# Kernel tuning notes

Measured on AMD Instinct MI355X. Metric: run time of the kernel, lower is better.

Reference implementation:

```python
import jax, jax.numpy as jnp
import numpy as np

MAX_K_QK = 64
MAX_K_V = 64
MAX_K_KNOW = 128


def threshold_gate(scores, tau, max_k):
    # scores: [B,S,N], tau: [B,S,1]
    raw = scores - tau
    gate = jnp.where(raw > 0, raw, 1e-08 * jnp.exp(raw))
    exp_gate = jnp.exp(gate) - 1.0
    k = min(max_k, scores.shape[-1])
    topk_vals, _ = jax.lax.top_k(exp_gate, k)
    threshold = topk_vals[:, :, -1:]
    exp_gate = jnp.where(exp_gate >= threshold, exp_gate, 0.0)
    gate_sum = exp_gate.sum(axis=-1, keepdims=True) + 1e-08
    gate_strength = jnp.tanh(exp_gate.max(axis=-1, keepdims=True))
    return exp_gate / gate_sum * gate_strength


def setup_inputs() -> dict:
    key = jax.random.key(0)
    ks = jax.random.split(key, 8)
    B, S, D = 2, 2048, 1024
    N_QK, N_V, N_KNOW = 4096, 4096, 8192
    scale = 0.02  # keep scores in a sane range for exp()
    return {
        "x": jax.random.normal(ks[0], (B, S, D), jnp.float32),
        "qk_emb": jax.random.normal(ks[1], (N_QK, D), jnp.float32) * scale,
        "v_emb": jax.random.normal(ks[2], (N_V, D), jnp.float32) * scale,
        "know_emb": jax.random.normal(ks[3], (N_KNOW, D), jnp.float32) * scale,
        "w_attn": jax.random.normal(ks[4], (D, 3), jnp.float32) * scale,
        "b_attn": jnp.zeros((3,), jnp.float32),
        "w_know": jax.random.normal(ks[5], (D, 1), jnp.float32) * scale,
        "b_know": jnp.zeros((1,), jnp.float32),
    }


def reference(x, qk_emb, v_emb, know_emb, w_attn, b_attn, w_know, b_know):
    # deterministic=True -> router dropout is identity
    # attention gates
    scores_qk = jnp.einsum("bsd,nd->bsn", x, qk_emb)
    scores_v = jnp.einsum("bsd,nd->bsn", x, v_emb)
    tau_all = x @ w_attn + b_attn  # [B,S,3]
    g_Q = threshold_gate(scores_qk, tau_all[:, :, 0:1], MAX_K_QK)
    g_K = threshold_gate(scores_qk, tau_all[:, :, 1:2], MAX_K_QK)
    g_V = threshold_gate(scores_v, tau_all[:, :, 2:3], MAX_K_V)
    t_qk = 1.0 / qk_emb.shape[0]
    t_v = 1.0 / v_emb.shape[0]
    aux_attn = (
        ((g_Q.mean(axis=(0, 1)) - t_qk) ** 2).sum() * g_Q.shape[-1]
        + ((g_K.mean(axis=(0, 1)) - t_qk) ** 2).sum() * g_K.shape[-1]
        + ((g_V.mean(axis=(0, 1)) - t_v) ** 2).sum() * g_V.shape[-1]
    )
    # knowledge gates
    scores_know = jnp.einsum("bsd,nd->bsn", x, know_emb)
    tau_know = x @ w_know + b_know  # [B,S,1]
    g_know = threshold_gate(scores_know, tau_know, MAX_K_KNOW)
    t_know = 1.0 / know_emb.shape[0]
    aux_know = ((g_know.mean(axis=(0, 1)) - t_know) ** 2).sum() * g_know.shape[-1]
    return (g_Q, g_K, g_V, aux_attn, g_know, aux_know)
```

## Files before the change

### kernel.cpp

```cpp
#include <hip/hip_runtime.h>
#include <hip/hip_bf16.h>


#define M_ROWS 4096
#define DIM    1024
#define N_QK   4096
#define N_KNOW 8192

typedef unsigned short ushortT;
typedef __attribute__((ext_vector_type(8)))  short short8;
typedef __attribute__((ext_vector_type(16))) float f32x16;

__global__ __launch_bounds__(256) void tau_kernel(
    const float* __restrict__ x, const float* __restrict__ w_attn,
    const float* __restrict__ b_attn, const float* __restrict__ w_know,
    const float* __restrict__ b_know, float* __restrict__ tau4, int D)
{
    __shared__ float s_f[4][4];
    const int row = blockIdx.x;
    const int tid = threadIdx.x;
    const float* xr = x + (size_t)row * D;
    float p0 = 0.f, p1 = 0.f, p2 = 0.f, p3 = 0.f;
    for (int d = tid; d < D; d += 256) {
        float xv = xr[d];
        p0 += xv * w_attn[d * 3 + 0];
        p1 += xv * w_attn[d * 3 + 1];
        p2 += xv * w_attn[d * 3 + 2];
        p3 += xv * w_know[d];
    }
#pragma unroll
    for (int o = 32; o > 0; o >>= 1) {
        p0 += __shfl_down(p0, o, 64);
        p1 += __shfl_down(p1, o, 64);
        p2 += __shfl_down(p2, o, 64);
        p3 += __shfl_down(p3, o, 64);
    }
    const int lane = tid & 63, wv = tid >> 6;
    if (lane == 0) { s_f[wv][0] = p0; s_f[wv][1] = p1; s_f[wv][2] = p2; s_f[wv][3] = p3; }
    __syncthreads();
    if (tid < 4) {
        float v = s_f[0][tid] + s_f[1][tid] + s_f[2][tid] + s_f[3][tid];
        v += (tid < 3) ? b_attn[tid] : b_know[0];
        tau4[(size_t)row * 4 + tid] = v;
    }
}

__device__ __forceinline__ void split4(const float4 v, uint2& H, uint2& L) {
    float vv[4] = {v.x, v.y, v.z, v.w};
    unsigned h[4], l[4];
#pragma unroll
    for (int i = 0; i < 4; i++) {
        __hip_bfloat16 hb = __float2bfloat16(vv[i]);
        float r = vv[i] - __bfloat162float(hb);
        __hip_bfloat16 lb = __float2bfloat16(r);
        h[i] = *(ushortT*)&hb;
        l[i] = *(ushortT*)&lb;
    }
    H.x = h[0] | (h[1] << 16); H.y = h[2] | (h[3] << 16);
    L.x = l[0] | (l[1] << 16); L.y = l[2] | (l[3] << 16);
}

__global__ __launch_bounds__(256) void convertA(
    const float* __restrict__ src, ushortT* __restrict__ dst, int nElem4)
{
    int g = blockIdx.x * 256 + threadIdx.x;
    if (g >= nElem4) return;
    int row = g >> 8;
    int c4  = g & 255;
    int chunk = c4 >> 3, pos = c4 & 7;
    const float4 v = *(const float4*)(src + (size_t)row * DIM + c4 * 4);
    uint2 H, L;
    split4(v, H, L);
    ushortT* base = dst + (size_t)row * 2048 + chunk * 64;
    *(uint2*)(base + pos * 4)      = H;
    *(uint2*)(base + 32 + pos * 4) = L;
}

__global__ __launch_bounds__(256) void gemm_fused3(
    const ushortT* __restrict__ Aext, const ushortT* __restrict__ Bext,
    float* __restrict__ gQ, float* __restrict__ gV, float* __restrict__ gKn,
    int nb0)
{
    __shared__ ushortT AHL[2][128 * 64];
    __shared__ ushortT BHL[2][128 * 64];
    const int tid = threadIdx.x;
    const int wave = tid >> 6, lane = tid & 63;
    const int l32 = lane & 31, h = lane >> 5;
    const int rx7 = l32 & 7;
    const int wm = (wave >> 1) * 64, wn = (wave & 1) * 64;
    const long long m0 = (long long)blockIdx.y * 128;
    const int nblk = nb0 + blockIdx.x;

    float* C; long long ldc; long long n0;
    if (nblk < 32)      { C = gQ;  ldc = N_QK;   n0 = (long long)nblk * 128; }
    else if (nblk < 64) { C = gV;  ldc = N_QK;   n0 = (long long)(nblk - 32) * 128; }
    else                { C = gKn; ldc = N_KNOW; n0 = (long long)(nblk - 64) * 128; }

    const ushortT* gAp[4]; const ushortT* gBp[4]; int lOff[4];
#pragma unroll
    for (int it = 0; it < 4; ++it) {
        int f = it * 256 + tid;
        int r = f >> 3, sp = f & 7;
        int sg = sp ^ (r & 7);
        gAp[it] = Aext + (m0 + r) * 2048 + sg * 8;
        gBp[it] = Bext + ((long long)blockIdx.x * 128 + r) * 2048 + sg * 8;
        lOff[it] = f * 8;
    }

    f32x16 acc[2][2] = {};

#define STAGE(buf, c) do {                                                         \
    _Pragma("unroll")                                                              \
    for (int it = 0; it < 4; ++it) {                                               \
        __builtin_amdgcn_global_load_lds(                                          \
            (const __attribute__((address_space(1))) unsigned*)(const void*)(gAp[it] + (c) * 64), \
            (__attribute__((address_space(3))) unsigned*)(void*)(&AHL[buf][0] + lOff[it]), 16, 0, 0); \
        __builtin_amdgcn_global_load_lds(                                          \
            (const __attribute__((address_space(1))) unsigned*)(const void*)(gBp[it] + (c) * 64), \
            (__attribute__((address_space(3))) unsigned*)(void*)(&BHL[buf][0] + lOff[it]), 16, 0, 0); \
    }                                                                              \
} while (0)

#define COMPUTE(buf) do {                                                          \
    _Pragma("unroll")                                                              \
    for (int kb = 0; kb < 2; ++kb) {                                               \
        const int so = ((kb * 2 + h) ^ rx7) * 16;                                  \
        short8 aH[2], aL[2], bH[2], bL[2];                                         \
        _Pragma("unroll")                                                          \
        for (int t = 0; t < 2; ++t) {                                              \
            const char* pa = (const char*)(&AHL[buf][0]) + (wm + t * 32 + l32) * 128; \
            const char* pb = (const char*)(&BHL[buf][0]) + (wn + t * 32 + l32) * 128; \
            aH[t] = *(const short8*)(pa + so);                                     \
            aL[t] = *(const short8*)(pa + (so ^ 64));                              \
            bH[t] = *(const short8*)(pb + so);                                     \
            bL[t] = *(const short8*)(pb + (so ^ 64));                              \
        }                                                                          \
        _Pragma("unroll")                                                          \
        for (int i = 0; i < 2; ++i)                                                \
            _Pragma("unroll")                                                      \
            for (int j = 0; j < 2; ++j)                                            \
                acc[i][j] = __builtin_amdgcn_mfma_f32_32x32x16_bf16(aH[i], bH[j], acc[i][j], 0, 0, 0); \
        _Pragma("unroll")                                                          \
        for (int i = 0; i < 2; ++i)                                                \
            _Pragma("unroll")                                                      \
            for (int j = 0; j < 2; ++j)                                            \
                acc[i][j] = __builtin_amdgcn_mfma_f32_32x32x16_bf16(aH[i], bL[j], acc[i][j], 0, 0, 0); \
        _Pragma("unroll")                                                          \
        for (int i = 0; i < 2; ++i)                                                \
            _Pragma("unroll")                                                      \
            for (int j = 0; j < 2; ++j)                                            \
                acc[i][j] = __builtin_amdgcn_mfma_f32_32x32x16_bf16(aL[i], bH[j], acc[i][j], 0, 0, 0); \
        _Pragma("unroll")                                                          \
        for (int i = 0; i < 2; ++i)                                                \
            _Pragma("unroll")                                                      \
            for (int j = 0; j < 2; ++j)                                            \
                acc[i][j] = __builtin_amdgcn_mfma_f32_32x32x16_bf16(aL[i], bL[j], acc[i][j], 0, 0, 0); \
    }                                                                              \
} while (0)

    STAGE(0, 0);
    __syncthreads();

    for (int c = 0; c < 32; c += 2) {
        STAGE(1, c + 1);
        COMPUTE(0);
        __syncthreads();
        if (c + 2 < 32) STAGE(0, c + 2);
        COMPUTE(1);
        __syncthreads();
    }
#undef STAGE
#undef COMPUTE

#pragma unroll
    for (int ti = 0; ti < 2; ++ti)
#pragma unroll
        for (int tj = 0; tj < 2; ++tj) {
            long long col = n0 + wn + tj * 32 + l32;
            long long rb  = m0 + wm + ti * 32 + 4 * h;
#pragma unroll
            for (int reg = 0; reg < 16; ++reg) {
                long long row = rb + (reg & 3) + 8 * (reg >> 2);
                C[row * ldc + col] = acc[ti][tj][reg];
            }
        }
}

__global__ __launch_bounds__(256) void gemm_fused2(
    const ushortT* __restrict__ Aext, const float* __restrict__ qk_emb,
    const float* __restrict__ v_emb, const float* __restrict__ know_emb,
    float* __restrict__ gQ, float* __restrict__ gV, float* __restrict__ gKn,
    long long rowOff)
{
    __shared__ ushortT AHL[128 * 64];
    __shared__ ushortT BHL[128 * 64];
    const int tid = threadIdx.x;
    const int wave = tid >> 6, lane = tid & 63;
    const int l32 = lane & 31, h = lane >> 5;
    const int rx7 = l32 & 7;
    const int wm = (wave >> 1) * 64, wn = (wave & 1) * 64;
    const long long m0 = (long long)blockIdx.y * 128;
    const int nblk = blockIdx.x;

    const float* Bsrc; float* C; long long ldc; long long n0;
    if (nblk < 32)      { Bsrc = qk_emb;   C = gQ;  ldc = N_QK;   n0 = (long long)nblk * 128; }
    else if (nblk < 64) { Bsrc = v_emb;    C = gV;  ldc = N_QK;   n0 = (long long)(nblk - 32) * 128; }
    else                { Bsrc = know_emb; C = gKn; ldc = N_KNOW; n0 = (long long)(nblk - 64) * 128; }

    const ushortT* gAp[4]; ushortT* lAp[4];
    const float*   gBp[4]; int offH[4], offL[4];
#pragma unroll
    for (int it = 0; it < 4; ++it) {
        int f = it * 256 + tid;
        int r = f >> 3, sp = f & 7;
        int sg = sp ^ (r & 7);
        gAp[it] = Aext + (m0 + r) * 2048 + sg * 8;
        lAp[it] = AHL + f * 8;
        int c4 = f & 7;
        int s = c4 >> 1, hf = c4 & 1;
        offH[it] = r * 128 + ((s ^ (r & 7)) * 16) + hf * 8;
        offL[it] = r * 128 + (((4 | s) ^ (r & 7)) * 16) + hf * 8;
        gBp[it] = Bsrc + (n0 + r) * DIM + c4 * 4;
    }
    const char* pA[2]; const char* pB[2];
#pragma unroll
    for (int t = 0; t < 2; ++t) {
        pA[t] = (const char*)AHL + (wm + t * 32 + l32) * 128;
        pB[t] = (const char*)BHL + (wn + t * 32 + l32) * 128;
    }

    f32x16 acc[2][2] = {};
    float4 bufB[4];
#pragma unroll
    for (int it = 0; it < 4; ++it) bufB[it] = *(const float4*)(gBp[it]);

    for (int c = 0; c < 32; ++c) {
#pragma unroll
        for (int it = 0; it < 4; ++it) {
            __builtin_amdgcn_global_load_lds(
                (const __attribute__((address_space(1))) unsigned*)(const void*)(gAp[it] + c * 64),
                (__attribute__((address_space(3))) unsigned*)(void*)lAp[it], 16, 0, 0);
            uint2 H, L;
            split4(bufB[it], H, L);
            *(uint2*)((char*)BHL + offH[it]) = H;
            *(uint2*)((char*)BHL + offL[it]) = L;
        }
        __syncthreads();
        if (c + 1 < 32) {
#pragma unroll
            for (int it = 0; it < 4; ++it)
                bufB[it] = *(const float4*)(gBp[it] + (c + 1) * 32);
        }
#pragma unroll
        for (int kb = 0; kb < 2; ++kb) {
            const int so = ((kb * 2 + h) ^ rx7) * 16;
            short8 aH[2], aL[2], bH[2], bL[2];
#pragma unroll
            for (int t = 0; t < 2; ++t) {
                aH[t] = *(const short8*)(pA[t] + so);
                aL[t] = *(const short8*)(pA[t] + (so ^ 64));
                bH[t] = *(const short8*)(pB[t] + so);
                bL[t] = *(const short8*)(pB[t] + (so ^ 64));
            }
#pragma unroll
            for (int i = 0; i < 2; ++i)
#pragma unroll
                for (int j = 0; j < 2; ++j) {
                    acc[i][j] = __builtin_amdgcn_mfma_f32_32x32x16_bf16(aH[i], bH[j], acc[i][j], 0, 0, 0);
                    acc[i][j] = __builtin_amdgcn_mfma_f32_32x32x16_bf16(aH[i], bL[j], acc[i][j], 0, 0, 0);
                    acc[i][j] = __builtin_amdgcn_mfma_f32_32x32x16_bf16(aL[i], bH[j], acc[i][j], 0, 0, 0);
                    acc[i][j] = __builtin_amdgcn_mfma_f32_32x32x16_bf16(aL[i], bL[j], acc[i][j], 0, 0, 0);
                }
        }
        __syncthreads();
    }
#pragma unroll
    for (int ti = 0; ti < 2; ++ti)
#pragma unroll
        for (int tj = 0; tj < 2; ++tj) {
            long long col = n0 + wn + tj * 32 + l32;
            long long rb  = rowOff + m0 + wm + ti * 32 + 4 * h;
#pragma unroll
            for (int reg = 0; reg < 16; ++reg) {
                long long row = rb + (reg & 3) + 8 * (reg >> 2);
                C[row * ldc + col] = acc[ti][tj][reg];
            }
        }
}

__device__ __forceinline__ unsigned floatToKey(float f) {
    unsigned b = __float_as_uint(f);
    return (b & 0x80000000u) ? ~b : (b | 0x80000000u);
}
__device__ __forceinline__ float keyToFloat(unsigned key) {
    unsigned b = (key & 0x80000000u) ? (key & 0x7FFFFFFFu) : ~key;
    return __uint_as_float(b);
}
__device__ __forceinline__ float egate(float raw) {
    float g = raw > 0.f ? raw : 1e-8f * __expf(raw);
    return expf(g) - 1.f;
}

template <int NV, bool VLOAD, bool VSTORE>
__device__ __forceinline__ void gate_body(
    const float* __restrict__ srow, float tA, float tB, bool hasB, int ksel,
    float* __restrict__ orowA, float* __restrict__ orowB,
    float* __restrict__ colA, float* __restrict__ colB,
    int* s_hist, unsigned* s_u, float* s_f)
{
    const int tid = threadIdx.x, lane = tid & 63, wv = tid >> 6;

    unsigned keys[NV * 4];
    unsigned kmax = 0u;
#pragma unroll
    for (int i = 0; i < NV; i++) {
        float v0, v1, v2, v3;
        if (VLOAD) {
            float4 v = *(const float4*)(srow + (size_t)(i * 256 + tid) * 4);
            v0 = v.x; v1 = v.y; v2 = v.z; v3 = v.w;
        } else {
            v0 = srow[(i * 4 + 0) * 256 + tid];
            v1 = srow[(i * 4 + 1) * 256 + tid];
            v2 = srow[(i * 4 + 2) * 256 + tid];
            v3 = srow[(i * 4 + 3) * 256 + tid];
        }
        unsigned a = floatToKey(v0), b = floatToKey(v1);
        unsigned c = floatToKey(v2), d = floatToKey(v3);
        keys[i * 4 + 0] = a; keys[i * 4 + 1] = b;
        keys[i * 4 + 2] = c; keys[i * 4 + 3] = d;
        unsigned m1 = a > b ? a : b, m2 = c > d ? c : d;
        m1 = m1 > m2 ? m1 : m2;
        kmax = kmax > m1 ? kmax : m1;
    }
#pragma unroll
    for (int o = 32; o > 0; o >>= 1) {
        unsigned x = __shfl_down(kmax, o, 64);
        kmax = kmax > x ? kmax : x;
    }
    if (lane == 0) s_u[wv] = kmax;
    __syncthreads();
    { unsigned a = s_u[0], b = s_u[1], c = s_u[2], d = s_u[3];
      unsigned m1 = a > b ? a : b, m2 = c > d ? c : d; kmax = m1 > m2 ? m1 : m2; }
    __syncthreads();

    unsigned prefix = 0u;
    int kk = ksel;
#pragma unroll
    for (int rnd = 0; rnd < 4; ++rnd) {
        const int sh = 24 - 8 * rnd;
        s_hist[tid] = 0;
        __syncthreads();
#pragma unroll
        for (int i = 0; i < NV * 4; i++) {
            unsigned key = keys[i];
            if ((((key ^ prefix) >> sh) >> 8) == 0u)
                atomicAdd(&s_hist[(key >> sh) & 255u], 1);
        }
        __syncthreads();
        if (tid < 64) {
            const int b3 = 255 - 4 * tid;
            const int h0 = s_hist[b3],     h1 = s_hist[b3 - 1];
            const int h2 = s_hist[b3 - 2], h3 = s_hist[b3 - 3];
            const int gsum = h0 + h1 + h2 + h3;
            int inc = gsum;
#pragma unroll
            for (int o = 1; o < 64; o <<= 1) {
                int v = __shfl_up(inc, o, 64);
                if (tid >= o) inc += v;
            }
            const int above = inc - gsum;
            const int c0 = above + h0, c1 = c0 + h1, c2 = c1 + h2, c3 = c2 + h3;
            if (kk > above && kk <= c3) {
                unsigned byt; int nk;
                if (kk <= c0)      { byt = (unsigned)b3;       nk = kk - above; }
                else if (kk <= c1) { byt = (unsigned)(b3 - 1); nk = kk - c0; }
                else if (kk <= c2) { byt = (unsigned)(b3 - 2); nk = kk - c1; }
                else               { byt = (unsigned)(b3 - 3); nk = kk - c2; }
                s_u[0] = byt; s_u[1] = (unsigned)nk;
            }
        }
        __syncthreads();
        prefix |= s_u[0] << sh;
        kk = (int)s_u[1];
    }
    const unsigned vk = prefix;

    float sA = 0.f, sB = 0.f;
#pragma unroll
    for (int i = 0; i < NV * 4; i++) {
        if (keys[i] >= vk) {
            float s = keyToFloat(keys[i]);
            sA += egate(s - tA);
            if (hasB) sB += egate(s - tB);
        }
    }
#pragma unroll
    for (int o = 32; o > 0; o >>= 1) {
        sA += __shfl_down(sA, o, 64);
        sB += __shfl_down(sB, o, 64);
    }
    if (lane == 0) { s_f[wv] = sA; s_f[4 + wv] = sB; }
    __syncthreads();
    sA = s_f[0] + s_f[1] + s_f[2] + s_f[3];
    sB = s_f[4] + s_f[5] + s_f[6] + s_f[7];

    const float smax = keyToFloat(kmax);
    const float scaleA = tanhf(egate(smax - tA)) / (sA + 1e-8f);
    const float scaleB = hasB ? tanhf(egate(smax - tB)) / (sB + 1e-8f) : 0.f;

#pragma unroll
    for (int i = 0; i < NV; i++) {
        float ga[4], gb[4];
        int eidx[4];
#pragma unroll
        for (int j = 0; j < 4; j++) {
            int ii = i * 4 + j;
            int idx = VLOAD ? (i * 1024 + tid * 4 + j) : (ii * 256 + tid);
            eidx[j] = idx;
            unsigned key = keys[ii];
            float vA = 0.f, vB = 0.f;
            if (key >= vk) {
                float s = keyToFloat(key);
                vA = egate(s - tA) * scaleA;
                atomicAdd(&colA[idx], vA);
                if (hasB) { vB = egate(s - tB) * scaleB; atomicAdd(&colB[idx], vB); }
            }
            ga[j] = vA; gb[j] = vB;
        }
        if (VSTORE) {
            *(float4*)(orowA + (size_t)eidx[0]) = make_float4(ga[0], ga[1], ga[2], ga[3]);
            if (hasB) *(float4*)(orowB + (size_t)eidx[0]) = make_float4(gb[0], gb[1], gb[2], gb[3]);
        } else {
#pragma unroll
            for (int j = 0; j < 4; j++) {
                orowA[eidx[j]] = ga[j];
                if (hasB) orowB[eidx[j]] = gb[j];
            }
        }
    }
}

__global__ __launch_bounds__(256) void gate_all(
    const float* __restrict__ tau4,
    float* __restrict__ gQ, float* __restrict__ gK,
    float* __restrict__ gV, float* __restrict__ gKn,
    float* __restrict__ colsums)
{
    __shared__ int s_hist[256];
    __shared__ unsigned s_u[4];
    __shared__ float s_f[8];
    const int bid = blockIdx.x;
    if (bid < 4096) {
        const int row = bid;
        const float t = tau4[(size_t)row * 4 + 3];
        gate_body<8, false, false>(
            gKn + (size_t)row * N_KNOW, t, 0.f, false, 128,
            gKn + (size_t)row * N_KNOW, nullptr,
            colsums + 3 * N_QK, nullptr, s_hist, s_u, s_f);
    } else if (bid < 8192) {
        const int row = bid - 4096;
        const float tA = tau4[(size_t)row * 4 + 0];
        const float tB = tau4[(size_t)row * 4 + 1];
        gate_body<4, true, true>(
            gQ + (size_t)row * N_QK, tA, tB, true, 64,
            gQ + (size_t)row * N_QK, gK + (size_t)row * N_QK,
            colsums, colsums + N_QK, s_hist, s_u, s_f);
    } else {
        const int row = bid - 8192;
        const float t = tau4[(size_t)row * 4 + 2];
        gate_body<4, true, true>(
            gV + (size_t)row * N_QK, t, 0.f, false, 64,
            gV + (size_t)row * N_QK, nullptr,
            colsums + 2 * N_QK, nullptr, s_hist, s_u, s_f);
    }
}

__global__ __launch_bounds__(256) void aux_kernel(
    const float* __restrict__ colsum,
    float* __restrict__ auxAttn, float* __restrict__ auxKnow)
{
    __shared__ float s_a[4];
    __shared__ float s_b[4];
    const int tid = threadIdx.x;
    const int lane = tid & 63, wv = tid >> 6;
    const float invM = 1.f / 4096.f;

    float sa = 0.f;
    const float tqk = 1.f / 4096.f;
    for (int i = tid; i < 3 * N_QK; i += 256) {
        float m = colsum[i] * invM - tqk;
        sa += m * m;
    }
    float sk = 0.f;
    const float tkn = 1.f / 8192.f;
    for (int i = tid; i < N_KNOW; i += 256) {
        float m = colsum[3 * N_QK + i] * invM - tkn;
        sk += m * m;
    }
#pragma unroll
    for (int o = 32; o > 0; o >>= 1) {
        sa += __shfl_down(sa, o, 64);
        sk += __shfl_down(sk, o, 64);
    }
    if (lane == 0) { s_a[wv] = sa; s_b[wv] = sk; }
    __syncthreads();
    if (tid == 0) {
        auxAttn[0] = (s_a[0] + s_a[1] + s_a[2] + s_a[3]) * 4096.f;
        auxKnow[0] = (s_b[0] + s_b[1] + s_b[2] + s_b[3]) * 8192.f;
    }
}

static void convert_b_range(const float* qk, const float* v, const float* kn,
                            ushortT* Bext, long long rowLo, long long rowHi,
                            hipStream_t stream)
{
    struct Seg { const float* p; long long lo, hi; };
    Seg seg[3] = { {qk, 0, 4096}, {v, 4096, 8192}, {kn, 8192, 16384} };
    for (int i = 0; i < 3; ++i) {
        long long lo = rowLo > seg[i].lo ? rowLo : seg[i].lo;
        long long hi = rowHi < seg[i].hi ? rowHi : seg[i].hi;
        if (lo < hi) {
            int nel4 = (int)((hi - lo) * 256);
            convertA<<<(nel4 + 255) / 256, 256, 0, stream>>>(
                seg[i].p + (size_t)(lo - seg[i].lo) * DIM,
                Bext + (size_t)(lo - rowLo) * 2048, nel4);
        }
    }
}

extern "C" void kernel_launch(void* const* d_in, const int* in_sizes, int n_in,
                              void* d_out, int out_size, void* d_ws, size_t ws_size,
                              hipStream_t stream)
{
    const float* x        = (const float*)d_in[0];
    const float* qk_emb   = (const float*)d_in[1];
    const float* v_emb    = (const float*)d_in[2];
    const float* know_emb = (const float*)d_in[3];
    const float* w_attn   = (const float*)d_in[4];
    const float* b_attn   = (const float*)d_in[5];
    const float* w_know   = (const float*)d_in[6];
    const float* b_know   = (const float*)d_in[7];
    float* out = (float*)d_out;

    const long long M = M_ROWS;

    float* gQ   = out;
    float* gK   = gQ + (size_t)M * N_QK;
    float* gV   = gK + (size_t)M * N_QK;
    float* auxA = gV + (size_t)M * N_QK;
    float* gKn  = auxA + 1;
    float* auxK = gKn + (size_t)M * N_KNOW;

    const long long nColsum = 3 * N_QK + N_KNOW;
    const long long tail_bytes = (M * 4 + nColsum) * 4;
    long long tailStart = ((long long)ws_size - tail_bytes) & ~255LL;
    float* tau4 = (float*)((char*)d_ws + tailStart);
    float* colsums = tau4 + (size_t)M * 4;

    const long long rowB = 4096;
    const long long aBytes = M * rowB;

    hipMemsetAsync(colsums, 0, nColsum * sizeof(float), stream);
    tau_kernel<<<(int)M, 256, 0, stream>>>(x, w_attn, b_attn, w_know, b_know, tau4, DIM);

    long long availB = tailStart - aBytes;
    long long nbc = availB > 0 ? availB / (128 * rowB) : 0;
    if (nbc > 128) nbc = 128;

    if (nbc >= 32) {
        ushortT* A_ext = (ushortT*)d_ws;
        ushortT* B_ext = (ushortT*)((char*)d_ws + aBytes);
        convertA<<<(int)(M * 256 / 256), 256, 0, stream>>>(x, A_ext, (int)(M * 256));
        for (long long nb0 = 0; nb0 < 128; nb0 += nbc) {
            long long nn = (128 - nb0 < nbc) ? (128 - nb0) : nbc;
            convert_b_range(qk_emb, v_emb, know_emb, B_ext,
                            nb0 * 128, (nb0 + nn) * 128, stream);
            gemm_fused3<<<dim3((unsigned)nn, 32), 256, 0, stream>>>(
                A_ext, B_ext, gQ, gV, gKn, (int)nb0);
        }
    } else {
        long long ra = (tailStart / rowB / 128) * 128;
        if (ra > M) ra = M;
        if (ra < 128) ra = 128;
        ushortT* A_ext = (ushortT*)d_ws;
        for (long long a0 = 0; a0 < M; a0 += ra) {
            long long ac = (M - a0 < ra) ? (M - a0) : ra;
            int nel4 = (int)(ac * 256);
            convertA<<<(nel4 + 255) / 256, 256, 0, stream>>>(x + a0 * DIM, A_ext, nel4);
            gemm_fused2<<<dim3(128, (unsigned)(ac / 128)), 256, 0, stream>>>(
                A_ext, qk_emb, v_emb, know_emb, gQ, gV, gKn, a0);
        }
    }

    gate_all<<<12288, 256, 0, stream>>>(tau4, gQ, gK, gV, gKn, colsums);

    aux_kernel<<<1, 256, 0, stream>>>(colsums, auxA, auxK);
}
```

Measured before the change: 1.058 ms.

## Enlarge fused GEMM tile to 256x256 with 512-thread blocks and dynamic LDS

Replaces the 128x128-tile, 256-thread split-bf16 GEMM with a 256x256-tile, 512-thread version. Each wave now computes 128x64 of output, and the double-buffered A/B stages move into 128 KB of dynamic shared memory. The aim is more reuse of each staged tile and fewer global/LDS loads per MFMA. In exchange it needs more registers and LDS per block, so fewer blocks run at once and the grid is smaller. The MFMA issue order now runs the four hi/lo products back-to-back on the same accumulator, which adds dependency chains unless the compiler reorders them.

```diff
diff --git a/kernel.cpp b/kernel.cpp
--- a/kernel.cpp
+++ b/kernel.cpp
@@ -76,48 +76,50 @@
     *(uint2*)(base + 32 + pos * 4) = L;
 }
 
-__global__ __launch_bounds__(256) void gemm_fused3(
+__global__ __launch_bounds__(512, 2) void gemm_fused4(
     const ushortT* __restrict__ Aext, const ushortT* __restrict__ Bext,
     float* __restrict__ gQ, float* __restrict__ gV, float* __restrict__ gKn,
     int nb0)
 {
-    __shared__ ushortT AHL[2][128 * 64];
-    __shared__ ushortT BHL[2][128 * 64];
+    extern __shared__ ushortT lds[];
+#define ABUF(b) (lds + (b) * 32768)
+#define BBUF(b) (lds + (b) * 32768 + 16384)
     const int tid = threadIdx.x;
     const int wave = tid >> 6, lane = tid & 63;
     const int l32 = lane & 31, h = lane >> 5;
     const int rx7 = l32 & 7;
-    const int wm = (wave >> 1) * 64, wn = (wave & 1) * 64;
-    const long long m0 = (long long)blockIdx.y * 128;
+    const int wm = (wave >> 2) * 128;
+    const int wn = (wave & 3) * 64;
+    const long long m0 = (long long)blockIdx.y * 256;
     const int nblk = nb0 + blockIdx.x;
 
     float* C; long long ldc; long long n0;
-    if (nblk < 32)      { C = gQ;  ldc = N_QK;   n0 = (long long)nblk * 128; }
-    else if (nblk < 64) { C = gV;  ldc = N_QK;   n0 = (long long)(nblk - 32) * 128; }
-    else                { C = gKn; ldc = N_KNOW; n0 = (long long)(nblk - 64) * 128; }
+    if (nblk < 16)      { C = gQ;  ldc = N_QK;   n0 = (long long)nblk * 256; }
+    else if (nblk < 32) { C = gV;  ldc = N_QK;   n0 = (long long)(nblk - 16) * 256; }
+    else                { C = gKn; ldc = N_KNOW; n0 = (long long)(nblk - 32) * 256; }
 
     const ushortT* gAp[4]; const ushortT* gBp[4]; int lOff[4];
 #pragma unroll
     for (int it = 0; it < 4; ++it) {
-        int f = it * 256 + tid;
+        int f = it * 512 + tid;
         int r = f >> 3, sp = f & 7;
         int sg = sp ^ (r & 7);
         gAp[it] = Aext + (m0 + r) * 2048 + sg * 8;
-        gBp[it] = Bext + ((long long)blockIdx.x * 128 + r) * 2048 + sg * 8;
+        gBp[it] = Bext + ((long long)blockIdx.x * 256 + r) * 2048 + sg * 8;
         lOff[it] = f * 8;
     }
 
-    f32x16 acc[2][2] = {};
+    f32x16 acc[4][2] = {};
 
 #define STAGE(buf, c) do {                                                         \
     _Pragma("unroll")                                                              \
     for (int it = 0; it < 4; ++it) {                                               \
         __builtin_amdgcn_global_load_lds(                                          \
             (const __attribute__((address_space(1))) unsigned*)(const void*)(gAp[it] + (c) * 64), \
-            (__attribute__((address_space(3))) unsigned*)(void*)(&AHL[buf][0] + lOff[it]), 16, 0, 0); \
+            (__attribute__((address_space(3))) unsigned*)(void*)(ABUF(buf) + lOff[it]), 16, 0, 0); \
         __builtin_amdgcn_global_load_lds(                                          \
             (const __attribute__((address_space(1))) unsigned*)(const void*)(gBp[it] + (c) * 64), \
-            (__attribute__((address_space(3))) unsigned*)(void*)(&BHL[buf][0] + lOff[it]), 16, 0, 0); \
+            (__attribute__((address_space(3))) unsigned*)(void*)(BBUF(buf) + lOff[it]), 16, 0, 0); \
     }                                                                              \
 } while (0)
 
@@ -125,36 +127,28 @@
     _Pragma("unroll")                                                              \
     for (int kb = 0; kb < 2; ++kb) {                                               \
         const int so = ((kb * 2 + h) ^ rx7) * 16;                                  \
-        short8 aH[2], aL[2], bH[2], bL[2];                                         \
+        short8 aH[4], aL[4], bH[2], bL[2];                                         \
+        _Pragma("unroll")                                                          \
+        for (int t = 0; t < 4; ++t) {                                              \
+            const char* pa = (const char*)ABUF(buf) + (wm + t * 32 + l32) * 128;   \
+            aH[t] = *(const short8*)(pa + so);                                     \
+            aL[t] = *(const short8*)(pa + (so ^ 64));                              \
+        }                                                                          \
         _Pragma("unroll")                                                          \
         for (int t = 0; t < 2; ++t) {                                              \
-            const char* pa = (const char*)(&AHL[buf][0]) + (wm + t * 32 + l32) * 128; \
-            const char* pb = (const char*)(&BHL[buf][0]) + (wn + t * 32 + l32) * 128; \
-            aH[t] = *(const short8*)(pa + so);                                     \
-            aL[t] = *(const short8*)(pa + (so ^ 64));                              \
+            const char* pb = (const char*)BBUF(buf) + (wn + t * 32 + l32) * 128;   \
             bH[t] = *(const short8*)(pb + so);                                     \
             bL[t] = *(const short8*)(pb + (so ^ 64));                              \
         }                                                                          \
         _Pragma("unroll")                                                          \
-        for (int i = 0; i < 2; ++i)                                                \
+        for (int i = 0; i < 4; ++i)                                                \
             _Pragma("unroll")                                                      \
-            for (int j = 0; j < 2; ++j)                                            \
+            for (int j = 0; j < 2; ++j) {                                          \
                 acc[i][j] = __builtin_amdgcn_mfma_f32_32x32x16_bf16(aH[i], bH[j], acc[i][j], 0, 0, 0); \
-        _Pragma("unroll")                                                          \
-        for (int i = 0; i < 2; ++i)                                                \
-            _Pragma("unroll")                                                      \
-            for (int j = 0; j < 2; ++j)                                            \
                 acc[i][j] = __builtin_amdgcn_mfma_f32_32x32x16_bf16(aH[i], bL[j], acc[i][j], 0, 0, 0); \
-        _Pragma("unroll")                                                          \
-        for (int i = 0; i < 2; ++i)                                                \
-            _Pragma("unroll")                                                      \
-            for (int j = 0; j < 2; ++j)                                            \
                 acc[i][j] = __builtin_amdgcn_mfma_f32_32x32x16_bf16(aL[i], bH[j], acc[i][j], 0, 0, 0); \
-        _Pragma("unroll")                                                          \
-        for (int i = 0; i < 2; ++i)                                                \
-            _Pragma("unroll")                                                      \
-            for (int j = 0; j < 2; ++j)                                            \
                 acc[i][j] = __builtin_amdgcn_mfma_f32_32x32x16_bf16(aL[i], bL[j], acc[i][j], 0, 0, 0); \
+            }                                                                      \
     }                                                                              \
 } while (0)
 
@@ -171,9 +165,11 @@
     }
 #undef STAGE
 #undef COMPUTE
-
-#pragma unroll
-    for (int ti = 0; ti < 2; ++ti)
+#undef ABUF
+#undef BBUF
+
+#pragma unroll
+    for (int ti = 0; ti < 4; ++ti)
 #pragma unroll
         for (int tj = 0; tj < 2; ++tj) {
             long long col = n0 + wn + tj * 32 + l32;
@@ -564,18 +560,18 @@
     tau_kernel<<<(int)M, 256, 0, stream>>>(x, w_attn, b_attn, w_know, b_know, tau4, DIM);
 
     long long availB = tailStart - aBytes;
-    long long nbc = availB > 0 ? availB / (128 * rowB) : 0;
-    if (nbc > 128) nbc = 128;
-
-    if (nbc >= 32) {
+    long long nbc = availB > 0 ? availB / (256 * rowB) : 0;
+    if (nbc > 64) nbc = 64;
+
+    if (nbc >= 16) {
         ushortT* A_ext = (ushortT*)d_ws;
         ushortT* B_ext = (ushortT*)((char*)d_ws + aBytes);
         convertA<<<(int)(M * 256 / 256), 256, 0, stream>>>(x, A_ext, (int)(M * 256));
-        for (long long nb0 = 0; nb0 < 128; nb0 += nbc) {
-            long long nn = (128 - nb0 < nbc) ? (128 - nb0) : nbc;
+        for (long long nb0 = 0; nb0 < 64; nb0 += nbc) {
+            long long nn = (64 - nb0 < nbc) ? (64 - nb0) : nbc;
             convert_b_range(qk_emb, v_emb, know_emb, B_ext,
-                            nb0 * 128, (nb0 + nn) * 128, stream);
-            gemm_fused3<<<dim3((unsigned)nn, 32), 256, 0, stream>>>(
+                            nb0 * 256, (nb0 + nn) * 256, stream);
+            gemm_fused4<<<dim3((unsigned)nn, 16), 512, 131072, stream>>>(
                 A_ext, B_ext, gQ, gV, gKn, (int)nb0);
         }
     } else {
```

Result: faster. 968.4 us (-8.5%).
